# Optimization experiments

Measured on AMD Instinct MI355X. Metric: run time of the kernel, lower is better.

Reference implementation:

```python
import jax, jax.numpy as jnp
import numpy as np

HIDDEN = 1024
N_EXPERTS = 8
TOP_K = 2
INTER = 1408
N_SHARED = 2
SCALE = 1.0  # routed_scaling_factor


def setup_inputs() -> dict:
    key = jax.random.key(0)
    ks = jax.random.split(key, 9)
    s_h = 1.0 / np.sqrt(HIDDEN)
    s_i = 1.0 / np.sqrt(INTER)
    x = jax.random.normal(ks[0], (2, 2048, HIDDEN), dtype=jnp.float32)
    gate_w = jax.random.uniform(ks[1], (N_EXPERTS, HIDDEN), jnp.float32, -s_h, s_h)  # kaiming_uniform-ish
    # routed experts: SwiGLU (gate, up, down), stacked over experts
    wg = jax.random.uniform(ks[2], (N_EXPERTS, HIDDEN, INTER), jnp.float32, -s_h, s_h)
    wu = jax.random.uniform(ks[3], (N_EXPERTS, HIDDEN, INTER), jnp.float32, -s_h, s_h)
    wd = jax.random.uniform(ks[4], (N_EXPERTS, INTER, HIDDEN), jnp.float32, -s_i, s_i)
    # shared experts: one SwiGLU with intermediate = INTER * N_SHARED
    si = INTER * N_SHARED
    s_si = 1.0 / np.sqrt(si)
    swg = jax.random.uniform(ks[5], (HIDDEN, si), jnp.float32, -s_h, s_h)
    swu = jax.random.uniform(ks[6], (HIDDEN, si), jnp.float32, -s_h, s_h)
    swd = jax.random.uniform(ks[7], (si, HIDDEN), jnp.float32, -s_si, s_si)
    return {"x": x, "gate_w": gate_w, "wg": wg, "wu": wu, "wd": wd,
            "swg": swg, "swu": swu, "swd": swd}


def reference(x, gate_w, wg, wu, wd, swg, swu, swd):
    B, S, H = x.shape
    xf = x.reshape(-1, H)                              # [T, H]
    T = xf.shape[0]
    # --- MoEGate (fp32) ---
    logits = xf.astype(jnp.float32) @ gate_w.astype(jnp.float32).T   # [T, E]
    scores = jax.nn.softmax(logits, axis=-1)
    topw, topi = jax.lax.top_k(scores, TOP_K)          # [T, K]
    denom = topw.sum(axis=-1, keepdims=True) + 1e-20   # norm_topk_prob (top_k > 1)
    topw = topw / denom * SCALE
    # dense combine weights [T, E]: zero except at top-k expert slots
    wdense = jnp.zeros((T, N_EXPERTS), jnp.float32).at[
        jnp.arange(T)[:, None], topi].set(topw)
    # --- routed experts (SwiGLU), computed densely per expert and combined ---
    hg = jnp.einsum('th,ehi->eti', xf, wg)             # [E, T, I]
    hu = jnp.einsum('th,ehi->eti', xf, wu)             # [E, T, I]
    eo = jnp.einsum('eti,eih->eth', jax.nn.silu(hg) * hu, wd)   # [E, T, H]
    y = jnp.einsum('te,eth->th', wdense, eo)           # weighted scatter-combine
    # --- shared experts ---
    shared = (jax.nn.silu(xf @ swg) * (xf @ swu)) @ swd
    return (y + shared).reshape(B, S, H)
```

## Files before the change

kernel.cpp:

```cpp
#include <hip/hip_runtime.h>
#include <hip/hip_bf16.h>
#include <math.h>

#define HIDDEN 1024
#define NEXP 8
#define TOPK 2
#define INTER 1408
#define SINTER 2816
#define NTOK 4096
#define NROWS (NTOK * TOPK)
#define NPANEL 10
#define TROWS 16384

typedef unsigned short ushort_t;
typedef __attribute__((ext_vector_type(8))) short short8;
typedef __attribute__((ext_vector_type(4))) float f32x4;

__device__ __forceinline__ ushort_t f2bf(float f) {
    unsigned int b = __float_as_uint(f);
    unsigned int r = (b + 0x7FFFu + ((b >> 16) & 1u)) >> 16;
    return (ushort_t)r;
}
__device__ __forceinline__ float silu_f(float g) {
    return g * (1.0f / (1.0f + __expf(-g)));
}

#define GLDS16(gp, lp) __builtin_amdgcn_global_load_lds(                     \
    (const __attribute__((address_space(1))) void*)(gp),                     \
    (__attribute__((address_space(3))) void*)(lp), 16, 0, 0)

__global__ void conv_x(const float* __restrict__ src, ushort_t* __restrict__ dst) {
    int i = (blockIdx.x * 256 + threadIdx.x) * 4;
    float4 v = *reinterpret_cast<const float4*>(&src[i]);
    union { ushort_t h[4]; unsigned long long ll; } p;
    p.h[0] = f2bf(v.x); p.h[1] = f2bf(v.y); p.h[2] = f2bf(v.z); p.h[3] = f2bf(v.w);
    *reinterpret_cast<unsigned long long*>(&dst[i]) = p.ll;
}

__global__ void tconv(const float* __restrict__ src, ushort_t* __restrict__ dst,
                      int R, int C, long sstride, long dstride) {
    src += (size_t)blockIdx.z * sstride;
    dst += (size_t)blockIdx.z * dstride;
    __shared__ float tile[32][33];
    int ct = blockIdx.x * 32, rt = blockIdx.y * 32;
    int tx = threadIdx.x, ty = threadIdx.y;
#pragma unroll
    for (int i = 0; i < 4; i++)
        tile[ty + 8 * i][tx] = src[(size_t)(rt + ty + 8 * i) * C + ct + tx];
    __syncthreads();
#pragma unroll
    for (int i = 0; i < 4; i++)
        dst[(size_t)(ct + ty + 8 * i) * R + rt + tx] = f2bf(tile[tx][ty + 8 * i]);
}

__global__ void gate_kernel(const float* __restrict__ x, const float* __restrict__ gw,
                            int* __restrict__ top_i, float* __restrict__ top_w) {
    int t = blockIdx.x;
    int lane = threadIdx.x;
    const float* xr = x + (size_t)t * HIDDEN;
    float acc[NEXP];
#pragma unroll
    for (int e = 0; e < NEXP; e++) acc[e] = 0.f;
    for (int j = 0; j < HIDDEN / 64; j++) {
        float xv = xr[lane + 64 * j];
#pragma unroll
        for (int e = 0; e < NEXP; e++)
            acc[e] = fmaf(xv, gw[e * HIDDEN + lane + 64 * j], acc[e]);
    }
#pragma unroll
    for (int e = 0; e < NEXP; e++) {
        float v = acc[e];
        for (int off = 32; off > 0; off >>= 1) v += __shfl_xor(v, off, 64);
        acc[e] = v;
    }
    if (lane == 0) {
        float mx = acc[0];
        for (int e = 1; e < NEXP; e++) mx = fmaxf(mx, acc[e]);
        float s[NEXP];
        float sum = 0.f;
        for (int e = 0; e < NEXP; e++) { s[e] = __expf(acc[e] - mx); sum += s[e]; }
        float inv = 1.0f / sum;
        for (int e = 0; e < NEXP; e++) s[e] *= inv;
        int e0 = 0;
        for (int e = 1; e < NEXP; e++) if (s[e] > s[e0]) e0 = e;
        int e1 = -1;
        for (int e = 0; e < NEXP; e++) {
            if (e == e0) continue;
            if (e1 < 0 || s[e] > s[e1]) e1 = e;
        }
        float w0 = s[e0], w1 = s[e1];
        float denom = w0 + w1 + 1e-20f;
        top_i[t * 2 + 0] = e0;
        top_i[t * 2 + 1] = e1;
        top_w[t * 2 + 0] = w0 / denom;
        top_w[t * 2 + 1] = w1 / denom;
    }
}

__global__ void assign_kernel(const int* __restrict__ top_i, int* __restrict__ cnt,
                              int* __restrict__ rnk) {
    int j = blockIdx.x * blockDim.x + threadIdx.x;
    if (j < NROWS) rnk[j] = atomicAdd(&cnt[top_i[j]], 1);
}

__global__ void scan_kernel(const int* __restrict__ cnt, int* __restrict__ offs2,
                            int* __restrict__ cnt2) {
    if (threadIdx.x == 0) {
        int o = 0;
        for (int e = 0; e < NEXP; e++) { offs2[e] = o; cnt2[e] = cnt[e]; o += cnt[e]; }
        offs2[8] = NROWS;          cnt2[8] = NTOK;
        offs2[9] = NROWS + NTOK;   cnt2[9] = NTOK;
        offs2[10] = TROWS;
    }
}

__global__ void fill_kernel(const int* __restrict__ top_i, const float* __restrict__ top_w,
                            const int* __restrict__ rnk, const int* __restrict__ offs2,
                            int* __restrict__ tok_of_row, float* __restrict__ w_of_row) {
    int j = blockIdx.x * blockDim.x + threadIdx.x;
    if (j < NROWS) {
        int row = offs2[top_i[j]] + rnk[j];
        tok_of_row[row] = j;
        w_of_row[row] = top_w[j];
    }
}

__global__ void fill_shared(int* __restrict__ tok_of_row, float* __restrict__ w_of_row) {
    int j = blockIdx.x * blockDim.x + threadIdx.x;
    int row = NROWS + j;
    tok_of_row[row] = (j & (NTOK - 1)) << 1;
    w_of_row[row] = 1.0f;
}

__global__ __launch_bounds__(256, 2) void gemm_gu(
    const ushort_t* __restrict__ xb, const ushort_t* __restrict__ WgT,
    const ushort_t* __restrict__ WuT, ushort_t* __restrict__ act,
    const int* __restrict__ tok_of_row, const int* __restrict__ offs2,
    const int* __restrict__ cnt2) {
    int e = blockIdx.z;
    int mcnt = cnt2[e];
    int m0 = blockIdx.y * 128;
    if (m0 >= mcnt) return;
    int base = offs2[e];
    int n0 = blockIdx.x * 128;
    const ushort_t* Bg = WgT + (size_t)e * INTER * HIDDEN;
    const ushort_t* Bu = WuT + (size_t)e * INTER * HIDDEN;

    __shared__ short As[128 * 32];
    __shared__ short Bgs[128 * 32];
    __shared__ short Bus[128 * 32];

    int tid = threadIdx.x;
    int wave = tid >> 6, lane = tid & 63;
    int wr = wave >> 1, wc = wave & 1;

    int srow0 = wave * 32 + (lane >> 2);
    int kq = (lane & 3) * 8;
    int r0 = m0 + srow0, r1 = r0 + 16;
    int rr0 = base + (r0 < mcnt ? r0 : mcnt - 1);
    int rr1 = base + (r1 < mcnt ? r1 : mcnt - 1);
    size_t tokA0 = (size_t)(tok_of_row[rr0] >> 1);
    size_t tokA1 = (size_t)(tok_of_row[rr1] >> 1);

    f32x4 accG[4][4] = {};
    f32x4 accU[4][4] = {};

    for (int k0 = 0; k0 < HIDDEN; k0 += 32) {
        GLDS16(xb + tokA0 * HIDDEN + k0 + kq, &As[wave * 1024]);
        GLDS16(xb + tokA1 * HIDDEN + k0 + kq, &As[wave * 1024 + 512]);
        GLDS16(Bg + (size_t)(n0 + srow0) * HIDDEN + k0 + kq, &Bgs[wave * 1024]);
        GLDS16(Bg + (size_t)(n0 + srow0 + 16) * HIDDEN + k0 + kq, &Bgs[wave * 1024 + 512]);
        GLDS16(Bu + (size_t)(n0 + srow0) * HIDDEN + k0 + kq, &Bus[wave * 1024]);
        GLDS16(Bu + (size_t)(n0 + srow0 + 16) * HIDDEN + k0 + kq, &Bus[wave * 1024 + 512]);
        __syncthreads();
        short8 a[4], bg[4], bu[4];
#pragma unroll
        for (int mi = 0; mi < 4; mi++)
            a[mi] = *reinterpret_cast<const short8*>(
                &As[(wr * 64 + mi * 16 + (lane & 15)) * 32 + (lane >> 4) * 8]);
#pragma unroll
        for (int ni = 0; ni < 4; ni++) {
            bg[ni] = *reinterpret_cast<const short8*>(
                &Bgs[(wc * 64 + ni * 16 + (lane & 15)) * 32 + (lane >> 4) * 8]);
            bu[ni] = *reinterpret_cast<const short8*>(
                &Bus[(wc * 64 + ni * 16 + (lane & 15)) * 32 + (lane >> 4) * 8]);
        }
#pragma unroll
        for (int mi = 0; mi < 4; mi++)
#pragma unroll
            for (int ni = 0; ni < 4; ni++) {
                accG[mi][ni] = __builtin_amdgcn_mfma_f32_16x16x32_bf16(
                    a[mi], bg[ni], accG[mi][ni], 0, 0, 0);
                accU[mi][ni] = __builtin_amdgcn_mfma_f32_16x16x32_bf16(
                    a[mi], bu[ni], accU[mi][ni], 0, 0, 0);
            }
        __syncthreads();
    }

#pragma unroll
    for (int mi = 0; mi < 4; mi++) {
#pragma unroll
        for (int ni = 0; ni < 4; ni++) {
            int col = n0 + wc * 64 + ni * 16 + (lane & 15);
#pragma unroll
            for (int r = 0; r < 4; r++) {
                int gm = m0 + wr * 64 + mi * 16 + (lane >> 4) * 4 + r;
                if (gm < mcnt) {
                    float g = accG[mi][ni][r], u = accU[mi][ni][r];
                    act[(size_t)(base + gm) * INTER + col] = f2bf(silu_f(g) * u);
                }
            }
        }
    }
}

__global__ __launch_bounds__(256, 2) void gemm_down(
    const ushort_t* __restrict__ act, const ushort_t* __restrict__ WdT,
    float* __restrict__ out, const int* __restrict__ tok_of_row,
    const float* __restrict__ w_of_row, const int* __restrict__ offs2,
    const int* __restrict__ cnt2) {
    int e = blockIdx.z;
    int mcnt = cnt2[e];
    int m0 = blockIdx.y * 128;
    if (m0 >= mcnt) return;
    int base = offs2[e];
    int n0 = blockIdx.x * 128;
    const ushort_t* Bd = WdT + (size_t)e * HIDDEN * INTER;

    __shared__ short As[128 * 32];
    __shared__ short Bs[128 * 32];

    int tid = threadIdx.x;
    int wave = tid >> 6, lane = tid & 63;
    int wr = wave >> 1, wc = wave & 1;

    int srow0 = wave * 32 + (lane >> 2);
    int kq = (lane & 3) * 8;
    size_t arow0 = (size_t)(base + m0 + srow0);
    size_t arow1 = arow0 + 16;

    f32x4 acc[4][4] = {};

    for (int k0 = 0; k0 < INTER; k0 += 32) {
        GLDS16(act + arow0 * INTER + k0 + kq, &As[wave * 1024]);
        GLDS16(act + arow1 * INTER + k0 + kq, &As[wave * 1024 + 512]);
        GLDS16(Bd + (size_t)(n0 + srow0) * INTER + k0 + kq, &Bs[wave * 1024]);
        GLDS16(Bd + (size_t)(n0 + srow0 + 16) * INTER + k0 + kq, &Bs[wave * 1024 + 512]);
        __syncthreads();
        short8 a[4], b[4];
#pragma unroll
        for (int mi = 0; mi < 4; mi++)
            a[mi] = *reinterpret_cast<const short8*>(
                &As[(wr * 64 + mi * 16 + (lane & 15)) * 32 + (lane >> 4) * 8]);
#pragma unroll
        for (int ni = 0; ni < 4; ni++)
            b[ni] = *reinterpret_cast<const short8*>(
                &Bs[(wc * 64 + ni * 16 + (lane & 15)) * 32 + (lane >> 4) * 8]);
#pragma unroll
        for (int mi = 0; mi < 4; mi++)
#pragma unroll
            for (int ni = 0; ni < 4; ni++)
                acc[mi][ni] = __builtin_amdgcn_mfma_f32_16x16x32_bf16(
                    a[mi], b[ni], acc[mi][ni], 0, 0, 0);
        __syncthreads();
    }

#pragma unroll
    for (int mi = 0; mi < 4; mi++) {
#pragma unroll
        for (int r = 0; r < 4; r++) {
            int gm = m0 + wr * 64 + mi * 16 + (lane >> 4) * 4 + r;
            if (gm < mcnt) {
                int tok = tok_of_row[base + gm] >> 1;
                float w = w_of_row[base + gm];
#pragma unroll
                for (int ni = 0; ni < 4; ni++) {
                    int col = n0 + wc * 64 + ni * 16 + (lane & 15);
                    atomicAdd(&out[(size_t)tok * HIDDEN + col], w * acc[mi][ni][r]);
                }
            }
        }
    }
}

extern "C" void kernel_launch(void* const* d_in, const int* in_sizes, int n_in,
                              void* d_out, int out_size, void* d_ws, size_t ws_size,
                              hipStream_t stream) {
    const float* x   = (const float*)d_in[0];
    const float* gw  = (const float*)d_in[1];
    const float* wg  = (const float*)d_in[2];
    const float* wu  = (const float*)d_in[3];
    const float* wd  = (const float*)d_in[4];
    const float* swg = (const float*)d_in[5];
    const float* swu = (const float*)d_in[6];
    const float* swd = (const float*)d_in[7];
    float* out = (float*)d_out;

    const size_t XB   = (size_t)NTOK * HIDDEN;
    const size_t WPAN = (size_t)NPANEL * INTER * HIDDEN;
    const size_t ACT  = (size_t)TROWS * INTER;
    ushort_t* xb  = (ushort_t*)d_ws;
    ushort_t* wgT = xb + XB;
    ushort_t* wuT = wgT + WPAN;
    ushort_t* wdT = wuT + WPAN;
    ushort_t* act = wdT + WPAN;
    int* ib = (int*)(act + ACT);
    int* top_i      = ib;
    int* rnk        = ib + NROWS;
    int* cnt        = ib + 2 * NROWS;
    int* offs2      = ib + 2 * NROWS + 8;
    int* cnt2       = offs2 + 16;
    int* tok_of_row = cnt2 + 16;
    float* top_w    = (float*)(tok_of_row + TROWS);
    float* w_of_row = top_w + NROWS;

    conv_x<<<(NTOK * HIDDEN) / (256 * 4), 256, 0, stream>>>(x, xb);
    dim3 tb(32, 8);
    tconv<<<dim3(INTER / 32, HIDDEN / 32, NEXP), tb, 0, stream>>>(
        wg, wgT, HIDDEN, INTER, (long)HIDDEN * INTER, (long)INTER * HIDDEN);
    tconv<<<dim3(INTER / 32, HIDDEN / 32, NEXP), tb, 0, stream>>>(
        wu, wuT, HIDDEN, INTER, (long)HIDDEN * INTER, (long)INTER * HIDDEN);
    tconv<<<dim3(SINTER / 32, HIDDEN / 32, 1), tb, 0, stream>>>(
        swg, wgT + (size_t)8 * INTER * HIDDEN, HIDDEN, SINTER, 0, 0);
    tconv<<<dim3(SINTER / 32, HIDDEN / 32, 1), tb, 0, stream>>>(
        swu, wuT + (size_t)8 * INTER * HIDDEN, HIDDEN, SINTER, 0, 0);
    tconv<<<dim3(HIDDEN / 32, INTER / 32, NEXP), tb, 0, stream>>>(
        wd, wdT, INTER, HIDDEN, (long)INTER * HIDDEN, (long)HIDDEN * INTER);
    tconv<<<dim3(HIDDEN / 32, INTER / 32, 2), tb, 0, stream>>>(
        swd, wdT + (size_t)8 * HIDDEN * INTER, INTER, HIDDEN,
        (long)INTER * HIDDEN, (long)HIDDEN * INTER);

    gate_kernel<<<NTOK, 64, 0, stream>>>(x, gw, top_i, top_w);
    hipMemsetAsync(cnt, 0, 8 * sizeof(int), stream);
    assign_kernel<<<NROWS / 256, 256, 0, stream>>>(top_i, cnt, rnk);
    scan_kernel<<<1, 1, 0, stream>>>(cnt, offs2, cnt2);
    fill_kernel<<<NROWS / 256, 256, 0, stream>>>(top_i, top_w, rnk, offs2,
                                                 tok_of_row, w_of_row);
    fill_shared<<<NROWS / 256, 256, 0, stream>>>(tok_of_row, w_of_row);

    gemm_gu<<<dim3(INTER / 128, 64, NPANEL), 256, 0, stream>>>(
        xb, wgT, wuT, act, tok_of_row, offs2, cnt2);
    hipMemsetAsync(out, 0, (size_t)out_size * sizeof(float), stream);
    gemm_down<<<dim3(HIDDEN / 128, 64, NPANEL), 256, 0, stream>>>(
        act, wdT, out, tok_of_row, w_of_row, offs2, cnt2);
}
```

Before: 389.8 us.

## Double-buffer LDS, widen MoE GEMM tiles to 256 rows, swizzle block order

Both grouped GEMMs now use 512-thread blocks with 256x128 tiles, double-buffered LDS staging and the next k-slice prefetched while MFMAs run on the current one. The LDS layout is changed to fragment-major so each lane reads its 16x32 slice contiguously. A block-index swizzle reorders the launch grid to change how blocks are spread across XCDs and how weights are reused in cache. The cost is lower occupancy (one large block per CU) and a full vmcnt(0) wait each iteration, which limits how much load latency the overlap can hide.

```diff
diff --git a/kernel.cpp b/kernel.cpp
--- a/kernel.cpp
+++ b/kernel.cpp
@@ -24,10 +24,23 @@
 __device__ __forceinline__ float silu_f(float g) {
     return g * (1.0f / (1.0f + __expf(-g)));
 }
+__device__ __forceinline__ int imin(int a, int b) { return a < b ? a : b; }
 
 #define GLDS16(gp, lp) __builtin_amdgcn_global_load_lds(                     \
     (const __attribute__((address_space(1))) void*)(gp),                     \
     (__attribute__((address_space(3))) void*)(lp), 16, 0, 0)
+
+__device__ __forceinline__ void swz3(int& bx, int& by, int& bz) {
+    int nb = gridDim.x, mb = gridDim.y;
+    int total = nb * mb * gridDim.z;
+    int orig = (blockIdx.z * mb + blockIdx.y) * nb + blockIdx.x;
+    int cpx = total >> 3;
+    int w = (orig & 7) * cpx + (orig >> 3);
+    bz = w / (nb * mb);
+    int rem = w - bz * (nb * mb);
+    by = rem / nb;
+    bx = rem - by * nb;
+}
 
 __global__ void conv_x(const float* __restrict__ src, ushort_t* __restrict__ dst) {
     int i = (blockIdx.x * 256 + threadIdx.x) * 4;
@@ -132,58 +145,71 @@
     w_of_row[row] = 1.0f;
 }
 
-__global__ __launch_bounds__(256, 2) void gemm_gu(
+__global__ __launch_bounds__(512, 1) void gemm_gu(
     const ushort_t* __restrict__ xb, const ushort_t* __restrict__ WgT,
     const ushort_t* __restrict__ WuT, ushort_t* __restrict__ act,
     const int* __restrict__ tok_of_row, const int* __restrict__ offs2,
     const int* __restrict__ cnt2) {
-    int e = blockIdx.z;
+    int bx, by, bz;
+    swz3(bx, by, bz);
+    int e = bz;
     int mcnt = cnt2[e];
-    int m0 = blockIdx.y * 128;
+    int m0 = by * 256;
     if (m0 >= mcnt) return;
     int base = offs2[e];
-    int n0 = blockIdx.x * 128;
+    int n0 = bx * 128;
     const ushort_t* Bg = WgT + (size_t)e * INTER * HIDDEN;
     const ushort_t* Bu = WuT + (size_t)e * INTER * HIDDEN;
 
-    __shared__ short As[128 * 32];
-    __shared__ short Bgs[128 * 32];
-    __shared__ short Bus[128 * 32];
+    __shared__ short As[2][16 * 512];
+    __shared__ short Bgs[2][8 * 512];
+    __shared__ short Bus[2][8 * 512];
 
     int tid = threadIdx.x;
     int wave = tid >> 6, lane = tid & 63;
     int wr = wave >> 1, wc = wave & 1;
-
-    int srow0 = wave * 32 + (lane >> 2);
-    int kq = (lane & 3) * 8;
-    int r0 = m0 + srow0, r1 = r0 + 16;
-    int rr0 = base + (r0 < mcnt ? r0 : mcnt - 1);
-    int rr1 = base + (r1 < mcnt ? r1 : mcnt - 1);
-    size_t tokA0 = (size_t)(tok_of_row[rr0] >> 1);
-    size_t tokA1 = (size_t)(tok_of_row[rr1] >> 1);
+    int lr = lane & 15;
+    int kq = (lane >> 4) * 8;
+
+    int ar0 = 2 * wave * 16 + lr;
+    int ar1 = ar0 + 16;
+    int rr0 = base + imin(m0 + ar0, mcnt - 1);
+    int rr1 = base + imin(m0 + ar1, mcnt - 1);
+    const ushort_t* srcA0 = xb + (size_t)(tok_of_row[rr0] >> 1) * HIDDEN + kq;
+    const ushort_t* srcA1 = xb + (size_t)(tok_of_row[rr1] >> 1) * HIDDEN + kq;
+    const ushort_t* srcBg = Bg + (size_t)(n0 + wave * 16 + lr) * HIDDEN + kq;
+    const ushort_t* srcBu = Bu + (size_t)(n0 + wave * 16 + lr) * HIDDEN + kq;
 
     f32x4 accG[4][4] = {};
     f32x4 accU[4][4] = {};
 
-    for (int k0 = 0; k0 < HIDDEN; k0 += 32) {
-        GLDS16(xb + tokA0 * HIDDEN + k0 + kq, &As[wave * 1024]);
-        GLDS16(xb + tokA1 * HIDDEN + k0 + kq, &As[wave * 1024 + 512]);
-        GLDS16(Bg + (size_t)(n0 + srow0) * HIDDEN + k0 + kq, &Bgs[wave * 1024]);
-        GLDS16(Bg + (size_t)(n0 + srow0 + 16) * HIDDEN + k0 + kq, &Bgs[wave * 1024 + 512]);
-        GLDS16(Bu + (size_t)(n0 + srow0) * HIDDEN + k0 + kq, &Bus[wave * 1024]);
-        GLDS16(Bu + (size_t)(n0 + srow0 + 16) * HIDDEN + k0 + kq, &Bus[wave * 1024 + 512]);
-        __syncthreads();
+#define STAGE_GU(buf, k0)                                                    \
+    do {                                                                     \
+        GLDS16(srcA0 + (k0), &As[buf][(2 * wave) * 512]);                    \
+        GLDS16(srcA1 + (k0), &As[buf][(2 * wave + 1) * 512]);                \
+        GLDS16(srcBg + (k0), &Bgs[buf][wave * 512]);                         \
+        GLDS16(srcBu + (k0), &Bus[buf][wave * 512]);                         \
+    } while (0)
+
+    STAGE_GU(0, 0);
+    asm volatile("s_waitcnt vmcnt(0)" ::: "memory");
+    __builtin_amdgcn_s_barrier();
+
+    const int NT = HIDDEN / 32;
+    int cur = 0;
+    for (int t = 0; t < NT; t++) {
+        if (t + 1 < NT) STAGE_GU(cur ^ 1, (t + 1) * 32);
         short8 a[4], bg[4], bu[4];
 #pragma unroll
         for (int mi = 0; mi < 4; mi++)
             a[mi] = *reinterpret_cast<const short8*>(
-                &As[(wr * 64 + mi * 16 + (lane & 15)) * 32 + (lane >> 4) * 8]);
+                &As[cur][(wr * 4 + mi) * 512 + lane * 8]);
 #pragma unroll
         for (int ni = 0; ni < 4; ni++) {
             bg[ni] = *reinterpret_cast<const short8*>(
-                &Bgs[(wc * 64 + ni * 16 + (lane & 15)) * 32 + (lane >> 4) * 8]);
+                &Bgs[cur][(wc * 4 + ni) * 512 + lane * 8]);
             bu[ni] = *reinterpret_cast<const short8*>(
-                &Bus[(wc * 64 + ni * 16 + (lane & 15)) * 32 + (lane >> 4) * 8]);
+                &Bus[cur][(wc * 4 + ni) * 512 + lane * 8]);
         }
 #pragma unroll
         for (int mi = 0; mi < 4; mi++)
@@ -194,14 +220,16 @@
                 accU[mi][ni] = __builtin_amdgcn_mfma_f32_16x16x32_bf16(
                     a[mi], bu[ni], accU[mi][ni], 0, 0, 0);
             }
-        __syncthreads();
+        asm volatile("s_waitcnt vmcnt(0)" ::: "memory");
+        __builtin_amdgcn_s_barrier();
+        cur ^= 1;
     }
 
 #pragma unroll
     for (int mi = 0; mi < 4; mi++) {
 #pragma unroll
         for (int ni = 0; ni < 4; ni++) {
-            int col = n0 + wc * 64 + ni * 16 + (lane & 15);
+            int col = n0 + wc * 64 + ni * 16 + lr;
 #pragma unroll
             for (int r = 0; r < 4; r++) {
                 int gm = m0 + wr * 64 + mi * 16 + (lane >> 4) * 4 + r;
@@ -212,57 +240,72 @@
             }
         }
     }
-}
-
-__global__ __launch_bounds__(256, 2) void gemm_down(
+#undef STAGE_GU
+}
+
+__global__ __launch_bounds__(512, 1) void gemm_down(
     const ushort_t* __restrict__ act, const ushort_t* __restrict__ WdT,
     float* __restrict__ out, const int* __restrict__ tok_of_row,
     const float* __restrict__ w_of_row, const int* __restrict__ offs2,
     const int* __restrict__ cnt2) {
-    int e = blockIdx.z;
+    int bx, by, bz;
+    swz3(bx, by, bz);
+    int e = bz;
     int mcnt = cnt2[e];
-    int m0 = blockIdx.y * 128;
+    int m0 = by * 256;
     if (m0 >= mcnt) return;
     int base = offs2[e];
-    int n0 = blockIdx.x * 128;
+    int n0 = bx * 128;
     const ushort_t* Bd = WdT + (size_t)e * HIDDEN * INTER;
 
-    __shared__ short As[128 * 32];
-    __shared__ short Bs[128 * 32];
+    __shared__ short As[2][16 * 512];
+    __shared__ short Bs[2][8 * 512];
 
     int tid = threadIdx.x;
     int wave = tid >> 6, lane = tid & 63;
     int wr = wave >> 1, wc = wave & 1;
-
-    int srow0 = wave * 32 + (lane >> 2);
-    int kq = (lane & 3) * 8;
-    size_t arow0 = (size_t)(base + m0 + srow0);
-    size_t arow1 = arow0 + 16;
+    int lr = lane & 15;
+    int kq = (lane >> 4) * 8;
+
+    const ushort_t* srcA0 = act + (size_t)(base + m0 + 2 * wave * 16 + lr) * INTER + kq;
+    const ushort_t* srcA1 = srcA0 + (size_t)16 * INTER;
+    const ushort_t* srcB = Bd + (size_t)(n0 + wave * 16 + lr) * INTER + kq;
 
     f32x4 acc[4][4] = {};
 
-    for (int k0 = 0; k0 < INTER; k0 += 32) {
-        GLDS16(act + arow0 * INTER + k0 + kq, &As[wave * 1024]);
-        GLDS16(act + arow1 * INTER + k0 + kq, &As[wave * 1024 + 512]);
-        GLDS16(Bd + (size_t)(n0 + srow0) * INTER + k0 + kq, &Bs[wave * 1024]);
-        GLDS16(Bd + (size_t)(n0 + srow0 + 16) * INTER + k0 + kq, &Bs[wave * 1024 + 512]);
-        __syncthreads();
+#define STAGE_D(buf, k0)                                                     \
+    do {                                                                     \
+        GLDS16(srcA0 + (k0), &As[buf][(2 * wave) * 512]);                    \
+        GLDS16(srcA1 + (k0), &As[buf][(2 * wave + 1) * 512]);                \
+        GLDS16(srcB + (k0), &Bs[buf][wave * 512]);                           \
+    } while (0)
+
+    STAGE_D(0, 0);
+    asm volatile("s_waitcnt vmcnt(0)" ::: "memory");
+    __builtin_amdgcn_s_barrier();
+
+    const int NT = INTER / 32;
+    int cur = 0;
+    for (int t = 0; t < NT; t++) {
+        if (t + 1 < NT) STAGE_D(cur ^ 1, (t + 1) * 32);
         short8 a[4], b[4];
 #pragma unroll
         for (int mi = 0; mi < 4; mi++)
             a[mi] = *reinterpret_cast<const short8*>(
-                &As[(wr * 64 + mi * 16 + (lane & 15)) * 32 + (lane >> 4) * 8]);
+                &As[cur][(wr * 4 + mi) * 512 + lane * 8]);
 #pragma unroll
         for (int ni = 0; ni < 4; ni++)
             b[ni] = *reinterpret_cast<const short8*>(
-                &Bs[(wc * 64 + ni * 16 + (lane & 15)) * 32 + (lane >> 4) * 8]);
+                &Bs[cur][(wc * 4 + ni) * 512 + lane * 8]);
 #pragma unroll
         for (int mi = 0; mi < 4; mi++)
 #pragma unroll
             for (int ni = 0; ni < 4; ni++)
                 acc[mi][ni] = __builtin_amdgcn_mfma_f32_16x16x32_bf16(
                     a[mi], b[ni], acc[mi][ni], 0, 0, 0);
-        __syncthreads();
+        asm volatile("s_waitcnt vmcnt(0)" ::: "memory");
+        __builtin_amdgcn_s_barrier();
+        cur ^= 1;
     }
 
 #pragma unroll
@@ -275,12 +318,13 @@
                 float w = w_of_row[base + gm];
 #pragma unroll
                 for (int ni = 0; ni < 4; ni++) {
-                    int col = n0 + wc * 64 + ni * 16 + (lane & 15);
+                    int col = n0 + wc * 64 + ni * 16 + lr;
                     atomicAdd(&out[(size_t)tok * HIDDEN + col], w * acc[mi][ni][r]);
                 }
             }
         }
     }
+#undef STAGE_D
 }
 
 extern "C" void kernel_launch(void* const* d_in, const int* in_sizes, int n_in,
@@ -338,9 +382,9 @@
                                                  tok_of_row, w_of_row);
     fill_shared<<<NROWS / 256, 256, 0, stream>>>(tok_of_row, w_of_row);
 
-    gemm_gu<<<dim3(INTER / 128, 64, NPANEL), 256, 0, stream>>>(
+    gemm_gu<<<dim3(INTER / 128, 32, NPANEL), 512, 0, stream>>>(
         xb, wgT, wuT, act, tok_of_row, offs2, cnt2);
     hipMemsetAsync(out, 0, (size_t)out_size * sizeof(float), stream);
-    gemm_down<<<dim3(HIDDEN / 128, 64, NPANEL), 256, 0, stream>>>(
+    gemm_down<<<dim3(HIDDEN / 128, 32, NPANEL), 512, 0, stream>>>(
         act, wdT, out, tok_of_row, w_of_row, offs2, cnt2);
 }
```

Result: slower. 596.6 us (+53.1%).
